# Optimization experiments

Measured on AMD Instinct MI355X. Metric: run time of the kernel, lower is better.

## Reference

```python
import jax, jax.numpy as jnp
import numpy as np

B, S, D = 8, 1024, 1024
H = 16
DH = D // H          # 64
F = 4096             # ffn_dims
EPS = 1e-6


def _dense_params(key, din, dout):
    kw, kb = jax.random.split(key)
    w = jax.random.normal(kw, (din, dout), jnp.float32) * (1.0 / np.sqrt(din))
    b = jnp.zeros((dout,), jnp.float32)
    return w, b


def setup_inputs() -> dict:
    key = jax.random.key(0)
    ks = jax.random.split(key, 8)
    x = jax.random.normal(ks[0], (B, S, D), jnp.float32)
    mask = jnp.zeros((B, 1, 1, S), jnp.float32)
    Wq, bq = _dense_params(ks[1], D, D)
    Wk, bk = _dense_params(ks[2], D, D)
    Wv, bv = _dense_params(ks[3], D, D)
    Wo, bo = _dense_params(ks[4], D, D)
    W1, bf1 = _dense_params(ks[5], D, F)
    W2, bf2 = _dense_params(ks[6], F, D)
    g1 = jnp.ones((D,), jnp.float32); be1 = jnp.zeros((D,), jnp.float32)
    g2 = jnp.ones((D,), jnp.float32); be2 = jnp.zeros((D,), jnp.float32)
    return dict(x=x, mask=mask, Wq=Wq, bq=bq, Wk=Wk, bk=bk, Wv=Wv, bv=bv,
                Wo=Wo, bo=bo, g1=g1, be1=be1, W1=W1, bf1=bf1, W2=W2, bf2=bf2,
                g2=g2, be2=be2)


def _layernorm(x, g, b):
    mu = jnp.mean(x, axis=-1, keepdims=True)
    var = jnp.mean(jnp.square(x - mu), axis=-1, keepdims=True)
    return g * (x - mu) * jax.lax.rsqrt(var + EPS) + b


def _split_heads(x):  # [B,S,D] -> [B,H,S,DH]
    return x.reshape(B, S, H, DH).transpose(0, 2, 1, 3)


def _encoder_block(x, mask, Wq, bq, Wk, bk, Wv, bv, Wo, bo,
                   g1, be1, W1, bf1, W2, bf2, g2, be2):
    q = _split_heads(x @ Wq + bq)
    k = _split_heads(x @ Wk + bk)
    v = _split_heads(x @ Wv + bv)
    scores = jnp.einsum('bhqd,bhkd->bhqk', q, k) / jnp.sqrt(jnp.float32(DH))
    scores = scores + mask * (-1e9)
    attn = jax.nn.softmax(scores, axis=-1)
    ctx = jnp.einsum('bhqk,bhkd->bhqd', attn, v)          # [B,H,S,DH]
    ctx = ctx.transpose(0, 2, 1, 3).reshape(B, S, D)      # merge heads
    y = ctx @ Wo + bo
    # dropout is identity at inference
    x1 = _layernorm(x + y, g1, be1)
    y2 = jax.nn.relu(x1 @ W1 + bf1) @ W2 + bf2
    return _layernorm(x1 + y2, g2, be2)


def reference(x, mask, Wq, bq, Wk, bk, Wv, bv, Wo, bo,
              g1, be1, W1, bf1, W2, bf2, g2, be2):
    return _encoder_block(x, mask, Wq, bq, Wk, bk, Wv, bv, Wo, bo,
                          g1, be1, W1, bf1, W2, bf2, g2, be2)
```

## Files before the change

kernel.cpp:

```cpp
#include <hip/hip_runtime.h>
#include <hip/hip_bf16.h>
#include <math.h>


typedef __hip_bfloat16 bf16;
typedef short bf16x8 __attribute__((ext_vector_type(8)));
typedef short bf16x4 __attribute__((ext_vector_type(4)));
typedef float f32x4 __attribute__((ext_vector_type(4)));

typedef unsigned int __attribute__((address_space(1))) as1_uint;
typedef unsigned int __attribute__((address_space(3))) as3_uint;

#define MFMA16(a, b, c) __builtin_amdgcn_mfma_f32_16x16x32_bf16((a), (b), (c), 0, 0, 0)
#define FLAG_RELU 1
#define FLAG_QKV 4
#define FLAG_OUTF32 8
#define SOFTMAX_SHIFT 20.0f
#define KSTRIDE 68
#define VSTRIDE 132

#define BAR() do { asm volatile("" ::: "memory"); \
    __builtin_amdgcn_s_barrier(); \
    asm volatile("" ::: "memory"); } while (0)
#define WAIT_LGKM0() do { asm volatile("s_waitcnt lgkmcnt(0)" ::: "memory"); \
    __builtin_amdgcn_sched_barrier(0); } while (0)
#define WAIT_VM4() do { asm volatile("s_waitcnt vmcnt(4)" ::: "memory"); \
    __builtin_amdgcn_sched_barrier(0); } while (0)
#define WAIT_VM0() do { asm volatile("s_waitcnt vmcnt(0)" ::: "memory"); \
    __builtin_amdgcn_sched_barrier(0); } while (0)

__device__ __forceinline__ float b2f(bf16 v) { return __bfloat162float(v); }
__device__ __forceinline__ bf16 f2b(float v) { return __float2bfloat16(v); }
__device__ __forceinline__ short f2bs(float v) {
    union { bf16 h; short s; } u;
    u.h = f2b(v);
    return u.s;
}
__device__ __forceinline__ float us2f(unsigned short u) {
    return __uint_as_float(((unsigned int)u) << 16);
}

__device__ __forceinline__ void async_copy16(void* lds, const void* gp) {
    __builtin_amdgcn_global_load_lds((const as1_uint*)gp, (as3_uint*)lds, 16, 0, 0);
}

__global__ void detect_k(const unsigned short* __restrict__ xs, int* flag) {
    __shared__ int vote;
    if (threadIdx.x == 0) vote = 0;
    __syncthreads();
    int bad = 0;
    for (int i = threadIdx.x; i < 16384; i += 256) {
        int e = (xs[i] >> 7) & 0xFF;
        if (e >= 0x84) bad = 1;
    }
    if (bad) atomicOr(&vote, 1);
    __syncthreads();
    if (threadIdx.x == 0) *flag = vote;
}

__global__ __launch_bounds__(256) void cvt_k(const void* __restrict__ in,
                                             bf16* __restrict__ out, int n,
                                             const int* __restrict__ flag) {
    const int f = *flag;
    const int base = (blockIdx.x * 256 + threadIdx.x) * 4;
    if (f) {
        const float* p = (const float*)in;
#pragma unroll
        for (int j = 0; j < 4; j++) {
            int i = base + j;
            if (i < n) out[i] = f2b(p[i]);
        }
    } else {
        const bf16* p = (const bf16*)in;
#pragma unroll
        for (int j = 0; j < 4; j++) {
            int i = base + j;
            if (i < n) out[i] = p[i];
        }
    }
}

struct CvtBatch {
    const void* src[11];
    bf16* dst[11];
    int n[11];
};
__global__ __launch_bounds__(256) void cvt_small_k(CvtBatch cb,
                                                   const int* __restrict__ flag) {
    const int f = *flag;
    const int seg = blockIdx.x;
    const int n = cb.n[seg];
    const void* in = cb.src[seg];
    bf16* out = cb.dst[seg];
    if (f) {
        const float* p = (const float*)in;
        for (int i = threadIdx.x; i < n; i += 256) out[i] = f2b(p[i]);
    } else {
        const bf16* p = (const bf16*)in;
        for (int i = threadIdx.x; i < n; i += 256) out[i] = p[i];
    }
}

__global__ __launch_bounds__(256) void transpose_k(const void* __restrict__ in,
                                                   bf16* __restrict__ out,
                                                   int R, int C,
                                                   const int* __restrict__ flag) {
    __shared__ bf16 tile[64][65];
    const int f = flag ? *flag : 0;
    const int tid = threadIdx.x;
    const size_t zoff = (size_t)blockIdx.z * R * C;
    const int tr = blockIdx.y * 64, tc = blockIdx.x * 64;
#pragma unroll
    for (int i = 0; i < 16; i++) {
        int idx = i * 256 + tid;
        int r = idx >> 6, c = idx & 63;
        size_t g = zoff + (size_t)(tr + r) * C + tc + c;
        tile[r][c] = f ? f2b(((const float*)in)[g]) : ((const bf16*)in)[g];
    }
    __syncthreads();
#pragma unroll
    for (int i = 0; i < 16; i++) {
        int idx = i * 256 + tid;
        int r = idx >> 6, c = idx & 63;
        out[zoff + (size_t)(tc + r) * R + tr + c] = tile[c][r];
    }
}

__global__ __launch_bounds__(512, 2) void gemm256(const bf16* __restrict__ A, int lda,
                                                  const bf16* __restrict__ Bt, int ldb,
                                                  const bf16* __restrict__ bias,
                                                  void* __restrict__ Cv, int ldc,
                                                  int M, int N, int K, int flags,
                                                  const int* __restrict__ dtf) {
    __shared__ __align__(16) bf16 As[2][256 * 64];
    __shared__ __align__(16) bf16 Bs[2][256 * 64];
    const int tid = threadIdx.x;
    const int wave = tid >> 6, lane = tid & 63;
    const int qd = lane >> 4, l15 = lane & 15;
    const int wm = wave >> 2, wn = wave & 3;

    const int NB = N >> 8;
    const int cpx = gridDim.x >> 3;
    const int swz = ((int)blockIdx.x & 7) * cpx + ((int)blockIdx.x >> 3);
    const int bn = swz % NB, bm = swz / NB;

    const int srow = tid >> 3;
    const int schunk = (tid & 7) ^ (srow & 7);
    const bf16* gA = A + (size_t)(bm * 256 + srow) * lda + schunk * 8;
    const bf16* gB = Bt + (size_t)(bn * 256 + srow) * ldb + schunk * 8;
    char* lA = (char*)As + wave * 1024;
    char* lB = (char*)Bs + wave * 1024;

    auto stA = [&](int d, int h, int tt) {
        const bf16* g = gA + (size_t)(h * 128) * lda + tt * 64;
        char* l = lA + d * 32768 + h * 16384;
        async_copy16(l, g);
        async_copy16(l + 8192, g + (size_t)64 * lda);
    };
    auto stB = [&](int d, int h, int tt) {
        const bf16* g = gB + (size_t)(h * 128) * ldb + tt * 64;
        char* l = lB + d * 32768 + h * 16384;
        async_copy16(l, g);
        async_copy16(l + 8192, g + (size_t)64 * ldb);
    };

    const int sx = l15 & 7;
    const char* pA = (const char*)As + (wm * 128 + l15) * 128;
    const char* pB = (const char*)Bs + (wn * 64 + l15) * 128;
    const int c0 = ((0 + qd) ^ sx) * 16;
    const int c1 = ((4 + qd) ^ sx) * 16;

    f32x4 acc[8][4] = {};
    bf16x8 af[4][2], bfr[4][2];
    const int nt = K >> 6;

    stA(0, 0, 0); stA(0, 1, 0); stB(0, 0, 0); stB(0, 1, 0);
    if (nt > 1) {
        stB(1, 0, 1); stA(1, 0, 1);
        WAIT_VM4();
    } else {
        WAIT_VM0();
    }
    BAR();

#pragma unroll 2
    for (int t = 0; t < nt; ++t) {
        const int d = t & 1, dn = d ^ 1;
        const int db = d * 32768;
#pragma unroll
        for (int m = 0; m < 4; ++m) {
            af[m][0] = *(const bf16x8*)(pA + db + m * 2048 + c0);
            af[m][1] = *(const bf16x8*)(pA + db + m * 2048 + c1);
        }
#pragma unroll
        for (int n = 0; n < 2; ++n) {
            bfr[n][0] = *(const bf16x8*)(pB + db + n * 2048 + c0);
            bfr[n][1] = *(const bf16x8*)(pB + db + n * 2048 + c1);
        }
        if (t + 1 < nt) stB(dn, 1, t + 1);
        BAR();
        WAIT_LGKM0();
        __builtin_amdgcn_s_setprio(1);
#pragma unroll
        for (int kk = 0; kk < 2; ++kk)
#pragma unroll
            for (int m = 0; m < 4; ++m)
#pragma unroll
                for (int n = 0; n < 2; ++n)
                    acc[m][n] = MFMA16(af[m][kk], bfr[n][kk], acc[m][n]);
        __builtin_amdgcn_s_setprio(0);
        BAR();
#pragma unroll
        for (int n = 0; n < 2; ++n) {
            bfr[2 + n][0] = *(const bf16x8*)(pB + db + (2 + n) * 2048 + c0);
            bfr[2 + n][1] = *(const bf16x8*)(pB + db + (2 + n) * 2048 + c1);
        }
        if (t + 1 < nt) stA(dn, 1, t + 1);
        BAR();
        WAIT_LGKM0();
        __builtin_amdgcn_s_setprio(1);
#pragma unroll
        for (int kk = 0; kk < 2; ++kk)
#pragma unroll
            for (int m = 0; m < 4; ++m)
#pragma unroll
                for (int n = 0; n < 2; ++n)
                    acc[m][2 + n] = MFMA16(af[m][kk], bfr[2 + n][kk], acc[m][2 + n]);
        __builtin_amdgcn_s_setprio(0);
        BAR();
#pragma unroll
        for (int m = 0; m < 4; ++m) {
            af[m][0] = *(const bf16x8*)(pA + db + (4 + m) * 2048 + c0);
            af[m][1] = *(const bf16x8*)(pA + db + (4 + m) * 2048 + c1);
        }
        if (t + 2 < nt) stB(d, 0, t + 2);
        BAR();
        WAIT_LGKM0();
        __builtin_amdgcn_s_setprio(1);
#pragma unroll
        for (int kk = 0; kk < 2; ++kk)
#pragma unroll
            for (int m = 0; m < 4; ++m)
#pragma unroll
                for (int n = 0; n < 2; ++n)
                    acc[4 + m][n] = MFMA16(af[m][kk], bfr[n][kk], acc[4 + m][n]);
        __builtin_amdgcn_s_setprio(0);
        BAR();
        if (t + 2 < nt) stA(d, 0, t + 2);
        BAR();
        __builtin_amdgcn_s_setprio(1);
#pragma unroll
        for (int kk = 0; kk < 2; ++kk)
#pragma unroll
            for (int m = 0; m < 4; ++m)
#pragma unroll
                for (int n = 0; n < 2; ++n)
                    acc[4 + m][2 + n] = MFMA16(af[m][kk], bfr[2 + n][kk], acc[4 + m][2 + n]);
        __builtin_amdgcn_s_setprio(0);
        if (t + 2 < nt) {
            WAIT_VM4();
        } else {
            WAIT_VM0();
        }
        BAR();
    }

    const int of32 = (flags & FLAG_OUTF32) ? *dtf : 0;
    bf16* C = (bf16*)Cv;
    float* Cf = (float*)Cv;
    float* ep = (float*)((char*)As + wave * 4352);
#pragma unroll
    for (int p = 0; p < 8; ++p) {
#pragma unroll
        for (int n = 0; n < 4; ++n)
#pragma unroll
            for (int r = 0; r < 4; ++r)
                ep[(qd * 4 + r) * 68 + n * 16 + l15] = acc[p][n][r];
        WAIT_LGKM0();
#pragma unroll
        for (int it = 0; it < 4; ++it) {
            const int idx = it * 64 + lane;
            const int row = idx >> 4;
            const int colc = (idx & 15) * 4;
            f32x4 v = *(const f32x4*)(ep + row * 68 + colc);
            const int gcol = bn * 256 + wn * 64 + colc;
            const bf16x4 bb = *(const bf16x4*)(bias + gcol);
            const int grow = bm * 256 + wm * 128 + p * 16 + row;
#pragma unroll
            for (int j = 0; j < 4; ++j) {
                float vv = v[j] + us2f((unsigned short)bb[j]);
                if (flags & FLAG_RELU) vv = fmaxf(vv, 0.f);
                v[j] = vv;
            }
            if (of32) {
                *(f32x4*)(Cf + (size_t)grow * ldc + gcol) = v;
            } else {
                const size_t cbase = (flags & FLAG_QKV)
                    ? (size_t)(gcol >> 10) * (8192u * 1024u) + (gcol & 1023)
                    : (size_t)gcol;
                bf16x4 h;
#pragma unroll
                for (int j = 0; j < 4; ++j) h[j] = f2bs(v[j]);
                *(bf16x4*)(C + (size_t)grow * ldc + cbase) = h;
            }
        }
        WAIT_LGKM0();
    }
}

__global__ __launch_bounds__(256) void attn_k(const bf16* __restrict__ Q,
                                              const bf16* __restrict__ Kc,
                                              const bf16* __restrict__ Vt,
                                              const bf16* __restrict__ mask,
                                              bf16* __restrict__ ctx) {
    const int S = 1024, D = 1024;
    __shared__ __align__(16) bf16 Ks[128 * KSTRIDE];
    __shared__ __align__(16) bf16 Vs[64 * VSTRIDE];
    const int tid = threadIdx.x, wave = tid >> 6, lane = tid & 63;
    const int qd = lane >> 4, l15 = lane & 15;
    const int qt = blockIdx.x, h = blockIdx.y, b = blockIdx.z;
    const size_t baseBSD = (size_t)b * S * D;

    const bf16* gK[4]; bf16* sK[4];
    const bf16* gV[4]; bf16* sV[4];
#pragma unroll
    for (int i = 0; i < 4; i++) {
        int t = tid + i * 256;
        gK[i] = Kc + baseBSD + (size_t)(t >> 3) * D + h * 64 + (t & 7) * 8;
        sK[i] = Ks + (t >> 3) * KSTRIDE + (t & 7) * 8;
        gV[i] = Vt + ((size_t)b * D + h * 64 + (t >> 4)) * S + (t & 15) * 8;
        sV[i] = Vs + (t >> 4) * VSTRIDE + (t & 15) * 8;
    }

    bf16x8 aq[2][2];
#pragma unroll
    for (int mt = 0; mt < 2; mt++)
#pragma unroll
        for (int ks = 0; ks < 2; ks++) {
            int row = qt * 128 + wave * 32 + mt * 16 + l15;
            int col = h * 64 + ks * 32 + qd * 8;
            aq[mt][ks] = *(const bf16x8*)(Q + baseBSD + (size_t)row * D + col);
        }

    bf16x8 kreg[4], vreg[4];
#pragma unroll
    for (int i = 0; i < 4; i++) {
        kreg[i] = *(const bf16x8*)(gK[i]);
        vreg[i] = *(const bf16x8*)(gV[i]);
    }

    f32x4 OT[2][4] = {};
    float lacc[2] = {0.f, 0.f};

    for (int kt = 0; kt < 8; kt++) {
        __syncthreads();
#pragma unroll
        for (int i = 0; i < 4; i++) {
            *(bf16x8*)sK[i] = kreg[i];
            *(bf16x8*)sV[i] = vreg[i];
        }
        __syncthreads();
        const int ktn = (kt < 7) ? kt + 1 : 7;
#pragma unroll
        for (int i = 0; i < 4; i++) {
            kreg[i] = *(const bf16x8*)(gK[i] + (size_t)ktn * 128 * D);
            vreg[i] = *(const bf16x8*)(gV[i] + ktn * 128);
        }
        bf16x8 pb[2][4];
#pragma unroll
        for (int g = 0; g < 2; g++) {
            f32x4 s[2][4] = {};
#pragma unroll
            for (int ks = 0; ks < 2; ks++) {
                bf16x8 ak[4];
#pragma unroll
                for (int n2 = 0; n2 < 4; n2++) {
                    int nt = g * 4 + n2;
                    ak[n2] = *(const bf16x8*)(Ks + (nt * 16 + l15) * KSTRIDE +
                                              ks * 32 + qd * 8);
                }
#pragma unroll
                for (int mt = 0; mt < 2; mt++)
#pragma unroll
                    for (int n2 = 0; n2 < 4; n2++)
                        s[mt][n2] = MFMA16(ak[n2], aq[mt][ks], s[mt][n2]);
            }
#pragma unroll
            for (int n2 = 0; n2 < 4; n2++) {
                int nt = g * 4 + n2;
                ushort4 mu = *(const ushort4*)(mask + b * S + kt * 128 +
                                               nt * 16 + qd * 4);
                float mv[4];
                mv[0] = fmaf(-1e9f, us2f(mu.x), -SOFTMAX_SHIFT);
                mv[1] = fmaf(-1e9f, us2f(mu.y), -SOFTMAX_SHIFT);
                mv[2] = fmaf(-1e9f, us2f(mu.z), -SOFTMAX_SHIFT);
                mv[3] = fmaf(-1e9f, us2f(mu.w), -SOFTMAX_SHIFT);
#pragma unroll
                for (int mt = 0; mt < 2; mt++)
#pragma unroll
                    for (int r = 0; r < 4; r++) {
                        float p = __expf(fmaf(s[mt][n2][r], 0.125f, mv[r]));
                        s[mt][n2][r] = p;
                        lacc[mt] += p;
                    }
            }
#pragma unroll
            for (int mt = 0; mt < 2; mt++)
#pragma unroll
                for (int half = 0; half < 2; half++) {
                    bf16x8 p8;
#pragma unroll
                    for (int j = 0; j < 4; j++) {
                        p8[j] = f2bs(s[mt][2 * half][j]);
                        p8[4 + j] = f2bs(s[mt][2 * half + 1][j]);
                    }
                    pb[mt][g * 2 + half] = p8;
                }
        }
#pragma unroll
        for (int c = 0; c < 4; c++) {
            bf16x8 av[4];
#pragma unroll
            for (int dt = 0; dt < 4; dt++) {
                const bf16* vb = Vs + (dt * 16 + l15) * VSTRIDE + qd * 4;
                bf16x4 lo = *(const bf16x4*)(vb + (2 * c) * 16);
                bf16x4 hi = *(const bf16x4*)(vb + (2 * c + 1) * 16);
                av[dt] = __builtin_shufflevector(lo, hi, 0, 1, 2, 3, 4, 5, 6, 7);
            }
#pragma unroll
            for (int mt = 0; mt < 2; mt++)
#pragma unroll
                for (int dt = 0; dt < 4; dt++)
                    OT[mt][dt] = MFMA16(av[dt], pb[mt][c], OT[mt][dt]);
        }
    }
#pragma unroll
    for (int mt = 0; mt < 2; mt++) {
        float rs = lacc[mt];
        rs += __shfl_xor(rs, 16);
        rs += __shfl_xor(rs, 32);
        const float inv = 1.f / rs;
        const int row = qt * 128 + wave * 32 + mt * 16 + l15;
#pragma unroll
        for (int dt = 0; dt < 4; dt++) {
            bf16x4 st;
#pragma unroll
            for (int r = 0; r < 4; r++) st[r] = f2bs(OT[mt][dt][r] * inv);
            *(bf16x4*)(ctx + baseBSD + (size_t)row * D + h * 64 + dt * 16 +
                       qd * 4) = st;
        }
    }
}

__global__ __launch_bounds__(256) void ln_add(const bf16* X,
                                              const bf16* __restrict__ Y,
                                              const bf16* __restrict__ g,
                                              const bf16* __restrict__ be,
                                              bf16* out) {
    const int tid = threadIdx.x;
    const int row = blockIdx.x;
    const size_t base = (size_t)row * 1024 + tid * 4;
    float v[4];
#pragma unroll
    for (int i = 0; i < 4; i++) v[i] = b2f(X[base + i]) + b2f(Y[base + i]);
    float s1 = 0.f, s2 = 0.f;
#pragma unroll
    for (int i = 0; i < 4; i++) {
        s1 += v[i];
        s2 += v[i] * v[i];
    }
    for (int off = 32; off; off >>= 1) {
        s1 += __shfl_xor(s1, off);
        s2 += __shfl_xor(s2, off);
    }
    __shared__ float red[8];
    const int wave = tid >> 6, lane = tid & 63;
    if (lane == 0) {
        red[wave] = s1;
        red[4 + wave] = s2;
    }
    __syncthreads();
    s1 = red[0] + red[1] + red[2] + red[3];
    s2 = red[4] + red[5] + red[6] + red[7];
    const float mu = s1 * (1.f / 1024.f);
    const float var = s2 * (1.f / 1024.f) - mu * mu;
    const float rstd = rsqrtf(var + 1e-6f);
    bf16 oh[4];
#pragma unroll
    for (int i = 0; i < 4; i++) {
        float gg = b2f(g[tid * 4 + i]);
        float bb = b2f(be[tid * 4 + i]);
        oh[i] = f2b(gg * (v[i] - mu) * rstd + bb);
    }
    *(ushort4*)(out + base) = *(ushort4*)oh;
}

__global__ __launch_bounds__(256) void ln_add_out(const bf16* __restrict__ X,
                                                  const void* Yv,
                                                  const bf16* __restrict__ g,
                                                  const bf16* __restrict__ be,
                                                  void* out,
                                                  const int* __restrict__ flag) {
    const int tid = threadIdx.x;
    const int row = blockIdx.x;
    const size_t base = (size_t)row * 1024 + tid * 4;
    const int f = *flag;
    float v[4];
    if (f) {
        float4 y = *(const float4*)((const float*)Yv + base);
        v[0] = b2f(X[base + 0]) + y.x;
        v[1] = b2f(X[base + 1]) + y.y;
        v[2] = b2f(X[base + 2]) + y.z;
        v[3] = b2f(X[base + 3]) + y.w;
    } else {
        const bf16* Yh = (const bf16*)Yv;
#pragma unroll
        for (int i = 0; i < 4; i++) v[i] = b2f(X[base + i]) + b2f(Yh[base + i]);
    }
    float s1 = 0.f, s2 = 0.f;
#pragma unroll
    for (int i = 0; i < 4; i++) {
        s1 += v[i];
        s2 += v[i] * v[i];
    }
    for (int off = 32; off; off >>= 1) {
        s1 += __shfl_xor(s1, off);
        s2 += __shfl_xor(s2, off);
    }
    __shared__ float red[8];
    const int wave = tid >> 6, lane = tid & 63;
    if (lane == 0) {
        red[wave] = s1;
        red[4 + wave] = s2;
    }
    __syncthreads();
    s1 = red[0] + red[1] + red[2] + red[3];
    s2 = red[4] + red[5] + red[6] + red[7];
    const float mu = s1 * (1.f / 1024.f);
    const float var = s2 * (1.f / 1024.f) - mu * mu;
    const float rstd = rsqrtf(var + 1e-6f);
    float o[4];
#pragma unroll
    for (int i = 0; i < 4; i++) {
        float gg = b2f(g[tid * 4 + i]);
        float bb = b2f(be[tid * 4 + i]);
        o[i] = gg * (v[i] - mu) * rstd + bb;
    }
    if (f) {
        *(float4*)((float*)out + base) = make_float4(o[0], o[1], o[2], o[3]);
    } else {
        bf16 oh[4];
#pragma unroll
        for (int i = 0; i < 4; i++) oh[i] = f2b(o[i]);
        *(ushort4*)((bf16*)out + base) = *(ushort4*)oh;
    }
}

extern "C" void kernel_launch(void* const* d_in, const int* in_sizes, int n_in,
                              void* d_out, int out_size, void* d_ws, size_t ws_size,
                              hipStream_t stream) {
    const void* x = d_in[0];
    const void* mask = d_in[1];
    const void* Wq = d_in[2];
    const void* bq = d_in[3];
    const void* Wk = d_in[4];
    const void* bk = d_in[5];
    const void* Wv = d_in[6];
    const void* bv = d_in[7];
    const void* Wo = d_in[8];
    const void* bo = d_in[9];
    const void* g1 = d_in[10];
    const void* be1 = d_in[11];
    const void* W1 = d_in[12];
    const void* bf1 = d_in[13];
    const void* W2 = d_in[14];
    const void* bf2 = d_in[15];
    const void* g2 = d_in[16];
    const void* be2 = d_in[17];

    char* ws = (char*)d_ws;
    const size_t MB = 1u << 20;
    const size_t KB = 1u << 10;
    bf16* WqkvT = (bf16*)(ws + 0 * MB);
    bf16* WoT = (bf16*)(ws + 6 * MB);
    bf16* xc = (bf16*)(ws + 8 * MB);
    bf16* Qb = (bf16*)(ws + 24 * MB);
    bf16* Kb = (bf16*)(ws + 40 * MB);
    bf16* Vb = (bf16*)(ws + 56 * MB);
    bf16* Vtb = (bf16*)(ws + 72 * MB);
    char* sm = ws + 88 * MB;
    int* flag = (int*)(sm + 0);
    bf16* mask_c = (bf16*)(sm + 4 * KB);
    bf16* bqkv_c = (bf16*)(sm + 20 * KB);
    bf16* bo_c = (bf16*)(sm + 26 * KB);
    bf16* bf1_c = (bf16*)(sm + 28 * KB);
    bf16* bf2_c = (bf16*)(sm + 36 * KB);
    bf16* g1_c = (bf16*)(sm + 38 * KB);
    bf16* be1_c = (bf16*)(sm + 40 * KB);
    bf16* g2_c = (bf16*)(sm + 42 * KB);
    bf16* be2_c = (bf16*)(sm + 44 * KB);
    bf16* yb = Qb;
    bf16* ctxb = Vb;
    bf16* x1b = xc;
    bf16* W1T = (bf16*)(ws + 0 * MB);
    bf16* W2T = (bf16*)(ws + 0 * MB);
    bf16* hb = Qb;

    dim3 blk(256);
    dim3 blk5(512);
    detect_k<<<dim3(1), blk, 0, stream>>>((const unsigned short*)x, flag);
    cvt_k<<<dim3(8192), blk, 0, stream>>>(x, xc, 8388608, flag);
    CvtBatch cb;
    cb.src[0] = mask;  cb.dst[0] = mask_c;        cb.n[0] = 8192;
    cb.src[1] = bq;    cb.dst[1] = bqkv_c;        cb.n[1] = 1024;
    cb.src[2] = bk;    cb.dst[2] = bqkv_c + 1024; cb.n[2] = 1024;
    cb.src[3] = bv;    cb.dst[3] = bqkv_c + 2048; cb.n[3] = 1024;
    cb.src[4] = bo;    cb.dst[4] = bo_c;          cb.n[4] = 1024;
    cb.src[5] = bf1;   cb.dst[5] = bf1_c;         cb.n[5] = 4096;
    cb.src[6] = bf2;   cb.dst[6] = bf2_c;         cb.n[6] = 1024;
    cb.src[7] = g1;    cb.dst[7] = g1_c;          cb.n[7] = 1024;
    cb.src[8] = be1;   cb.dst[8] = be1_c;         cb.n[8] = 1024;
    cb.src[9] = g2;    cb.dst[9] = g2_c;          cb.n[9] = 1024;
    cb.src[10] = be2;  cb.dst[10] = be2_c;        cb.n[10] = 1024;
    cvt_small_k<<<dim3(11), blk, 0, stream>>>(cb, flag);
    transpose_k<<<dim3(16, 16, 1), blk, 0, stream>>>(Wq, WqkvT, 1024, 1024, flag);
    transpose_k<<<dim3(16, 16, 1), blk, 0, stream>>>(Wk, WqkvT + 1024 * 1024, 1024, 1024, flag);
    transpose_k<<<dim3(16, 16, 1), blk, 0, stream>>>(Wv, WqkvT + 2048 * 1024, 1024, 1024, flag);
    transpose_k<<<dim3(16, 16, 1), blk, 0, stream>>>(Wo, WoT, 1024, 1024, flag);
    gemm256<<<dim3(384), blk5, 0, stream>>>(xc, 1024, WqkvT, 1024, bqkv_c, Qb, 1024, 8192, 3072, 1024, FLAG_QKV, nullptr);
    transpose_k<<<dim3(16, 16, 8), blk, 0, stream>>>(Vb, Vtb, 1024, 1024, nullptr);
    attn_k<<<dim3(8, 16, 8), blk, 0, stream>>>(Qb, Kb, Vtb, mask_c, ctxb);
    gemm256<<<dim3(128), blk5, 0, stream>>>(ctxb, 1024, WoT, 1024, bo_c, yb, 1024, 8192, 1024, 1024, 0, nullptr);
    ln_add<<<dim3(8192), blk, 0, stream>>>(xc, yb, g1_c, be1_c, x1b);
    transpose_k<<<dim3(64, 16, 1), blk, 0, stream>>>(W1, W1T, 1024, 4096, flag);
    gemm256<<<dim3(512), blk5, 0, stream>>>(x1b, 1024, W1T, 1024, bf1_c, hb, 4096, 8192, 4096, 1024, FLAG_RELU, nullptr);
    transpose_k<<<dim3(16, 64, 1), blk, 0, stream>>>(W2, W2T, 4096, 1024, flag);
    gemm256<<<dim3(128), blk5, 0, stream>>>(hb, 4096, W2T, 4096, bf2_c, d_out, 1024, 8192, 1024, 4096, FLAG_OUTF32, flag);
    ln_add_out<<<dim3(8192), blk, 0, stream>>>(x1b, d_out, g2_c, be2_c, d_out, flag);
}
```

Measured before the change: 636.7 us.

## Split-K the two N=1024 GEMMs and fold partial sums into layernorm

Adds a split-K mode to the 256x256 GEMM. The output-projection and FFN-down GEMMs now launch 256 blocks instead of 128, each block computing half of K and writing fp32 partials to two buffers. New layernorm kernels sum the two partials with the residual, so no separate reduction kernel is needed. The aim is better occupancy on a GPU with more CUs than 128 tiles can fill. The cost is extra fp32 traffic for the partials, and the split path runs only when the workspace is large enough.

After: 605.9 us. 1.05x faster.

```diff
diff --git a/kernel.cpp b/kernel.cpp
--- a/kernel.cpp
+++ b/kernel.cpp
@@ -15,6 +15,7 @@
 #define FLAG_RELU 1
 #define FLAG_QKV 4
 #define FLAG_OUTF32 8
+#define FLAG_SPLITK 16
 #define SOFTMAX_SHIFT 20.0f
 #define KSTRIDE 68
 #define VSTRIDE 132
@@ -131,7 +132,8 @@
                                                   const bf16* __restrict__ bias,
                                                   void* __restrict__ Cv, int ldc,
                                                   int M, int N, int K, int flags,
-                                                  const int* __restrict__ dtf) {
+                                                  const int* __restrict__ dtf,
+                                                  void* __restrict__ Cv2) {
     __shared__ __align__(16) bf16 As[2][256 * 64];
     __shared__ __align__(16) bf16 Bs[2][256 * 64];
     const int tid = threadIdx.x;
@@ -142,12 +144,17 @@
     const int NB = N >> 8;
     const int cpx = gridDim.x >> 3;
     const int swz = ((int)blockIdx.x & 7) * cpx + ((int)blockIdx.x >> 3);
-    const int bn = swz % NB, bm = swz / NB;
+    const int splitk = flags & FLAG_SPLITK;
+    const int kpart = splitk ? (swz & 1) : 0;
+    const int tileIdx = splitk ? (swz >> 1) : swz;
+    const int bn = tileIdx % NB, bm = tileIdx / NB;
+    const int Keff = splitk ? (K >> 1) : K;
+    const int koff = kpart ? Keff : 0;
 
     const int srow = tid >> 3;
     const int schunk = (tid & 7) ^ (srow & 7);
-    const bf16* gA = A + (size_t)(bm * 256 + srow) * lda + schunk * 8;
-    const bf16* gB = Bt + (size_t)(bn * 256 + srow) * ldb + schunk * 8;
+    const bf16* gA = A + (size_t)(bm * 256 + srow) * lda + koff + schunk * 8;
+    const bf16* gB = Bt + (size_t)(bn * 256 + srow) * ldb + koff + schunk * 8;
     char* lA = (char*)As + wave * 1024;
     char* lB = (char*)Bs + wave * 1024;
 
@@ -172,7 +179,7 @@
 
     f32x4 acc[8][4] = {};
     bf16x8 af[4][2], bfr[4][2];
-    const int nt = K >> 6;
+    const int nt = Keff >> 6;
 
     stA(0, 0, 0); stA(0, 1, 0); stB(0, 0, 0); stB(0, 1, 0);
     if (nt > 1) {
@@ -267,7 +274,7 @@
 
     const int of32 = (flags & FLAG_OUTF32) ? *dtf : 0;
     bf16* C = (bf16*)Cv;
-    float* Cf = (float*)Cv;
+    float* Cf = (float*)(kpart ? Cv2 : Cv);
     float* ep = (float*)((char*)As + wave * 4352);
 #pragma unroll
     for (int p = 0; p < 8; ++p) {
@@ -288,11 +295,12 @@
             const int grow = bm * 256 + wm * 128 + p * 16 + row;
 #pragma unroll
             for (int j = 0; j < 4; ++j) {
-                float vv = v[j] + us2f((unsigned short)bb[j]);
+                float bvj = (kpart == 0) ? us2f((unsigned short)bb[j]) : 0.f;
+                float vv = v[j] + bvj;
                 if (flags & FLAG_RELU) vv = fmaxf(vv, 0.f);
                 v[j] = vv;
             }
-            if (of32) {
+            if (splitk || of32) {
                 *(f32x4*)(Cf + (size_t)grow * ldc + gcol) = v;
             } else {
                 const size_t cbase = (flags & FLAG_QKV)
@@ -463,6 +471,54 @@
     float v[4];
 #pragma unroll
     for (int i = 0; i < 4; i++) v[i] = b2f(X[base + i]) + b2f(Y[base + i]);
+    float s1 = 0.f, s2 = 0.f;
+#pragma unroll
+    for (int i = 0; i < 4; i++) {
+        s1 += v[i];
+        s2 += v[i] * v[i];
+    }
+    for (int off = 32; off; off >>= 1) {
+        s1 += __shfl_xor(s1, off);
+        s2 += __shfl_xor(s2, off);
+    }
+    __shared__ float red[8];
+    const int wave = tid >> 6, lane = tid & 63;
+    if (lane == 0) {
+        red[wave] = s1;
+        red[4 + wave] = s2;
+    }
+    __syncthreads();
+    s1 = red[0] + red[1] + red[2] + red[3];
+    s2 = red[4] + red[5] + red[6] + red[7];
+    const float mu = s1 * (1.f / 1024.f);
+    const float var = s2 * (1.f / 1024.f) - mu * mu;
+    const float rstd = rsqrtf(var + 1e-6f);
+    bf16 oh[4];
+#pragma unroll
+    for (int i = 0; i < 4; i++) {
+        float gg = b2f(g[tid * 4 + i]);
+        float bb = b2f(be[tid * 4 + i]);
+        oh[i] = f2b(gg * (v[i] - mu) * rstd + bb);
+    }
+    *(ushort4*)(out + base) = *(ushort4*)oh;
+}
+
+__global__ __launch_bounds__(256) void ln_add2f(const bf16* X,
+                                                const float* __restrict__ P0,
+                                                const float* __restrict__ P1,
+                                                const bf16* __restrict__ g,
+                                                const bf16* __restrict__ be,
+                                                bf16* out) {
+    const int tid = threadIdx.x;
+    const int row = blockIdx.x;
+    const size_t base = (size_t)row * 1024 + tid * 4;
+    float4 p0 = *(const float4*)(P0 + base);
+    float4 p1 = *(const float4*)(P1 + base);
+    float v[4];
+    v[0] = b2f(X[base + 0]) + p0.x + p1.x;
+    v[1] = b2f(X[base + 1]) + p0.y + p1.y;
+    v[2] = b2f(X[base + 2]) + p0.z + p1.z;
+    v[3] = b2f(X[base + 3]) + p0.w + p1.w;
     float s1 = 0.f, s2 = 0.f;
 #pragma unroll
     for (int i = 0; i < 4; i++) {
@@ -517,6 +573,63 @@
 #pragma unroll
         for (int i = 0; i < 4; i++) v[i] = b2f(X[base + i]) + b2f(Yh[base + i]);
     }
+    float s1 = 0.f, s2 = 0.f;
+#pragma unroll
+    for (int i = 0; i < 4; i++) {
+        s1 += v[i];
+        s2 += v[i] * v[i];
+    }
+    for (int off = 32; off; off >>= 1) {
+        s1 += __shfl_xor(s1, off);
+        s2 += __shfl_xor(s2, off);
+    }
+    __shared__ float red[8];
+    const int wave = tid >> 6, lane = tid & 63;
+    if (lane == 0) {
+        red[wave] = s1;
+        red[4 + wave] = s2;
+    }
+    __syncthreads();
+    s1 = red[0] + red[1] + red[2] + red[3];
+    s2 = red[4] + red[5] + red[6] + red[7];
+    const float mu = s1 * (1.f / 1024.f);
+    const float var = s2 * (1.f / 1024.f) - mu * mu;
+    const float rstd = rsqrtf(var + 1e-6f);
+    float o[4];
+#pragma unroll
+    for (int i = 0; i < 4; i++) {
+        float gg = b2f(g[tid * 4 + i]);
+        float bb = b2f(be[tid * 4 + i]);
+        o[i] = gg * (v[i] - mu) * rstd + bb;
+    }
+    if (f) {
+        *(float4*)((float*)out + base) = make_float4(o[0], o[1], o[2], o[3]);
+    } else {
+        bf16 oh[4];
+#pragma unroll
+        for (int i = 0; i < 4; i++) oh[i] = f2b(o[i]);
+        *(ushort4*)((bf16*)out + base) = *(ushort4*)oh;
+    }
+}
+
+__global__ __launch_bounds__(256) void ln_add_out2f(const bf16* __restrict__ X,
+                                                    const float* P0,
+                                                    const float* __restrict__ P1,
+                                                    const bf16* __restrict__ g,
+                                                    const bf16* __restrict__ be,
+                                                    void* out,
+                                                    const int* __restrict__ flag) {
+    const int tid = threadIdx.x;
+    const int row = blockIdx.x;
+    const size_t base = (size_t)row * 1024 + tid * 4;
+    const int f = *flag;
+    float4 p0 = *(const float4*)(P0 + base);
+    float4 p1 = *(const float4*)(P1 + base);
+    float v[4];
+    v[0] = b2f(X[base + 0]) + p0.x + p1.x;
+    v[1] = b2f(X[base + 1]) + p0.y + p1.y;
+    v[2] = b2f(X[base + 2]) + p0.z + p1.z;
+    v[3] = b2f(X[base + 3]) + p0.w + p1.w;
     float s1 = 0.f, s2 = 0.f;
 #pragma unroll
     for (int i = 0; i < 4; i++) {
@@ -605,6 +718,12 @@
     bf16* W1T = (bf16*)(ws + 0 * MB);
     bf16* W2T = (bf16*)(ws + 0 * MB);
     bf16* hb = Qb;
+    float* pk1 = (float*)(ws + 89 * MB);
+    float* yw0 = (float*)Qb;
+    const bool f32out = (out_size >= 32 * 1024 * 1024);
+    float* p0f = f32out ? (float*)d_out : (float*)(ws + 121 * MB);
+    const size_t need_ws = f32out ? 121 * MB + 32 * MB : 153 * MB + 32 * MB;
+    const bool do_split = (ws_size >= need_ws);
 
     dim3 blk(256);
     dim3 blk5(512);
@@ -627,14 +746,24 @@
     transpose_k<<<dim3(16, 16, 1), blk, 0, stream>>>(Wk, WqkvT + 1024 * 1024, 1024, 1024, flag);
     transpose_k<<<dim3(16, 16, 1), blk, 0, stream>>>(Wv, WqkvT + 2048 * 1024, 1024, 1024, flag);
     transpose_k<<<dim3(16, 16, 1), blk, 0, stream>>>(Wo, WoT, 1024, 1024, flag);
-    gemm256<<<dim3(384), blk5, 0, stream>>>(xc, 1024, WqkvT, 1024, bqkv_c, Qb, 1024, 8192, 3072, 1024, FLAG_QKV, nullptr);
+    gemm256<<<dim3(384), blk5, 0, stream>>>(xc, 1024, WqkvT, 1024, bqkv_c, Qb, 1024, 8192, 3072, 1024, FLAG_QKV, nullptr, nullptr);
     transpose_k<<<dim3(16, 16, 8), blk, 0, stream>>>(Vb, Vtb, 1024, 1024, nullptr);
     attn_k<<<dim3(8, 16, 8), blk, 0, stream>>>(Qb, Kb, Vtb, mask_c, ctxb);
-    gemm256<<<dim3(128), blk5, 0, stream>>>(ctxb, 1024, WoT, 1024, bo_c, yb, 1024, 8192, 1024, 1024, 0, nullptr);
-    ln_add<<<dim3(8192), blk, 0, stream>>>(xc, yb, g1_c, be1_c, x1b);
+    if (do_split) {
+        gemm256<<<dim3(256), blk5, 0, stream>>>(ctxb, 1024, WoT, 1024, bo_c, yw0, 1024, 8192, 1024, 1024, FLAG_SPLITK, nullptr, pk1);
+        ln_add2f<<<dim3(8192), blk, 0, stream>>>(xc, yw0, pk1, g1_c, be1_c, x1b);
+    } else {
+        gemm256<<<dim3(128), blk5, 0, stream>>>(ctxb, 1024, WoT, 1024, bo_c, yb, 1024, 8192, 1024, 1024, 0, nullptr, nullptr);
+        ln_add<<<dim3(8192), blk, 0, stream>>>(xc, yb, g1_c, be1_c, x1b);
+    }
     transpose_k<<<dim3(64, 16, 1), blk, 0, stream>>>(W1, W1T, 1024, 4096, flag);
-    gemm256<<<dim3(512), blk5, 0, stream>>>(x1b, 1024, W1T, 1024, bf1_c, hb, 4096, 8192, 4096, 1024, FLAG_RELU, nullptr);
+    gemm256<<<dim3(512), blk5, 0, stream>>>(x1b, 1024, W1T, 1024, bf1_c, hb, 4096, 8192, 4096, 1024, FLAG_RELU, nullptr, nullptr);
     transpose_k<<<dim3(16, 64, 1), blk, 0, stream>>>(W2, W2T, 4096, 1024, flag);
-    gemm256<<<dim3(128), blk5, 0, stream>>>(hb, 4096, W2T, 4096, bf2_c, d_out, 1024, 8192, 1024, 4096, FLAG_OUTF32, flag);
-    ln_add_out<<<dim3(8192), blk, 0, stream>>>(x1b, d_out, g2_c, be2_c, d_out, flag);
-}
+    if (do_split) {
+        gemm256<<<dim3(256), blk5, 0, stream>>>(hb, 4096, W2T, 4096, bf2_c, p0f, 1024, 8192, 1024, 4096, FLAG_SPLITK, nullptr, pk1);
+        ln_add_out2f<<<dim3(8192), blk, 0, stream>>>(x1b, p0f, pk1, g2_c, be2_c, d_out, flag);
+    } else {
+        gemm256<<<dim3(128), blk5, 0, stream>>>(hb, 4096, W2T, 4096, bf2_c, d_out, 1024, 8192, 1024, 4096, FLAG_OUTF32, flag, nullptr);
+        ln_add_out<<<dim3(8192), blk, 0, stream>>>(x1b, d_out, g2_c, be2_c, d_out, flag);
+    }
+}
```
